# Performance work log

Hardware: AMD Instinct MI355X
Metric: run time of the kernel (lower is better)

The kernel has to match this reference:

```python
import jax, jax.numpy as jnp
import numpy as np
from jax import lax

B, T, IN, H, OUT = 4096, 512, 2, 12, 2


def setup_inputs() -> dict:
    key = jax.random.key(0)
    ks = jax.random.split(key, 11)
    s = 1.0 / np.sqrt(H)  # PyTorch LSTM init scale
    f32 = jnp.float32
    return {
        "x": jax.random.normal(ks[0], (B, T, IN), dtype=f32),
        "W_ih0": jax.random.uniform(ks[1], (4 * H, IN), dtype=f32, minval=-s, maxval=s),
        "W_hh0": jax.random.uniform(ks[2], (4 * H, H), dtype=f32, minval=-s, maxval=s),
        "b_ih0": jax.random.uniform(ks[3], (4 * H,), dtype=f32, minval=-s, maxval=s),
        "b_hh0": jax.random.uniform(ks[4], (4 * H,), dtype=f32, minval=-s, maxval=s),
        "W_ih1": jax.random.uniform(ks[5], (4 * H, H), dtype=f32, minval=-s, maxval=s),
        "W_hh1": jax.random.uniform(ks[6], (4 * H, H), dtype=f32, minval=-s, maxval=s),
        "b_ih1": jax.random.uniform(ks[7], (4 * H,), dtype=f32, minval=-s, maxval=s),
        "b_hh1": jax.random.uniform(ks[8], (4 * H,), dtype=f32, minval=-s, maxval=s),
        "fc_W": jax.random.uniform(ks[9], (OUT, H), dtype=f32, minval=-s, maxval=s),
        "fc_b": jax.random.uniform(ks[10], (OUT,), dtype=f32, minval=-s, maxval=s),
    }


def _lstm_layer(x, W_ih, W_hh, b_ih, b_hh):
    # x: [B, T, in_dim] -> hidden trajectory [B, T, H]
    b, h = x.shape[0], W_hh.shape[1]
    # Precompute input contribution for all timesteps: [T, B, 4H]
    xg = jnp.einsum('bti,gi->tbg', x, W_ih) + b_ih + b_hh

    def step(carry, xg_t):
        hprev, cprev = carry
        gates = xg_t + hprev @ W_hh.T  # [B, 4H], PyTorch gate order i,f,g,o
        i, f, g, o = jnp.split(gates, 4, axis=-1)
        i = jax.nn.sigmoid(i)
        f = jax.nn.sigmoid(f)
        g = jnp.tanh(g)
        o = jax.nn.sigmoid(o)
        c = f * cprev + i * g
        hnew = o * jnp.tanh(c)
        return (hnew, c), hnew

    z = jnp.zeros((b, h), dtype=x.dtype)
    _, hs = lax.scan(step, (z, z), xg)  # hs: [T, B, H]
    return jnp.swapaxes(hs, 0, 1)  # [B, T, H]


def reference(x, W_ih0, W_hh0, b_ih0, b_hh0, W_ih1, W_hh1, b_ih1, b_hh1, fc_W, fc_b):
    # 2-layer LSTM, h0=c0=0; dropout is identity in eval mode.
    h1 = _lstm_layer(x, W_ih0, W_hh0, b_ih0, b_hh0)   # [B, T, H]
    h2 = _lstm_layer(h1, W_ih1, W_hh1, b_ih1, b_hh1)  # [B, T, H]
    last = h2[:, -1, :]                               # [B, H]
    return last @ fc_W.T + fc_b                       # [B, OUT]
```

## Files before the change

kernel.cpp:

```cpp
#include <hip/hip_runtime.h>


namespace {
constexpr int H = 12;
constexpr int T = 512;
constexpr float LOG2E = 1.4426950408889634f;

__device__ __forceinline__ float exp2_(float x) {
    float r; asm("v_exp_f32 %0, %1" : "=v"(r) : "v"(x)); return r;
}
__device__ __forceinline__ float rcp_(float x) { return __builtin_amdgcn_rcpf(x); }
template <int CTRL>
__device__ __forceinline__ float mdpp(float v) {
    return __int_as_float(__builtin_amdgcn_mov_dpp(
        __float_as_int(v), CTRL, 0xF, 0xF, true));
}
constexpr int BC1 = 0x55;
constexpr int BC2 = 0xAA;
constexpr int BC3 = 0xFF;

__device__ __forceinline__ float tanh_(float c) {
    return fmaf(2.0f, rcp_(1.0f + exp2_(-2.0f * LOG2E * c)), -1.0f);
}
}

__global__ __launch_bounds__(512, 8) void lstm2_fc_kernel(
    const float* __restrict__ x,
    const float* __restrict__ W_ih0,
    const float* __restrict__ W_hh0,
    const float* __restrict__ b_ih0,
    const float* __restrict__ b_hh0,
    const float* __restrict__ W_ih1,
    const float* __restrict__ W_hh1,
    const float* __restrict__ b_ih1,
    const float* __restrict__ b_hh1,
    const float* __restrict__ fc_W,
    const float* __restrict__ fc_b,
    float* __restrict__ out)
{
    const int tid  = threadIdx.x;
    const int lane = tid & 63;
    const int wv   = __builtin_amdgcn_readfirstlane(tid >> 6);
    const bool L1w = (wv >= 4);
    const int ew   = wv & 3;
    const int b    = blockIdx.x * 4 + ew;
    const int u    = lane >> 2;
    const int gate = lane & 3;
    const int uc   = (u < H) ? u : 0;
    const int r    = gate * H + uc;

    const float pre  = (gate == 2) ? 2.0f : 1.0f;
    const float kmul = -LOG2E * pre;
    const float pa   = 1.0f - pre;

    __shared__ float sm[4 * 64];
    float* eb = &sm[ew * 64];
    const bool pub = (gate == 0) && (u < H);

    float w[24];
    float bias;
    if (!L1w) {
        w[0] = kmul * W_ih0[r * 2 + 0];
        w[1] = kmul * W_ih0[r * 2 + 1];
#pragma unroll
        for (int j = 0; j < H; ++j) w[2 + j] = kmul * W_hh0[r * H + j];
#pragma unroll
        for (int j = 0; j < 10; ++j) w[14 + j] = 0.0f;
        bias = kmul * (b_ih0[r] + b_hh0[r]);
    } else {
#pragma unroll
        for (int j = 0; j < H; ++j) {
            w[j]      = kmul * W_ih1[r * H + j];
            w[12 + j] = kmul * W_hh1[r * H + j];
        }
        bias = kmul * (b_ih1[r] + b_hh1[r]);
    }

    float c = 0.0f;
    float hb[H];
#pragma unroll
    for (int j = 0; j < H; ++j) hb[j] = 0.0f;

    const float* xp = x + (size_t)b * T * 2;
    float2 xc = *(const float2*)xp;

    for (int t = 0; t <= T; ++t) {
        if (!L1w) {
            if (t < T) {
                const int tn = (t < T - 1) ? (t + 1) : t;
                const float2 xn = *(const float2*)(xp + 2 * tn);
                float a = fmaf(w[0], xc.x, bias);
                a = fmaf(w[1], xc.y, a);
#pragma unroll
                for (int j = 0; j < H; ++j) a = fmaf(w[2 + j], hb[j], a);
                const float s = fmaf(pre, rcp_(1.0f + exp2_(a)), pa);
                const float F = mdpp<BC1>(s);
                const float G = mdpp<BC2>(s);
                const float O = mdpp<BC3>(s);
                c = fmaf(F, c, s * G);
                const float hv = O * tanh_(c);
                float* buf = eb + (t & 1) * 16;
                if (pub) buf[uc] = hv;
#pragma unroll
                for (int j = 0; j < H; ++j) hb[j] = buf[j];
                xc = xn;
            }
        } else {
            if (t > 0) {
                const int s0 = t - 1;
                const float* h0buf = eb + (s0 & 1) * 16;
                float a = bias;
#pragma unroll
                for (int j = 0; j < H; ++j) a = fmaf(w[12 + j], hb[j], a);
#pragma unroll
                for (int j = 0; j < H; ++j) a = fmaf(w[j], h0buf[j], a);
                const float sg = fmaf(pre, rcp_(1.0f + exp2_(a)), pa);
                const float F = mdpp<BC1>(sg);
                const float G = mdpp<BC2>(sg);
                const float O = mdpp<BC3>(sg);
                c = fmaf(F, c, sg * G);
                const float hv = O * tanh_(c);
                if (pub) eb[32 + uc] = hv;
#pragma unroll
                for (int j = 0; j < H; ++j) hb[j] = eb[32 + j];
            }
        }
        __syncthreads();
    }

    if (L1w && lane == 0) {
        float r0 = fc_b[0];
        float r1 = fc_b[1];
#pragma unroll
        for (int j = 0; j < H; ++j) {
            r0 = fmaf(fc_W[j],     hb[j], r0);
            r1 = fmaf(fc_W[H + j], hb[j], r1);
        }
        float2 res; res.x = r0; res.y = r1;
        *(float2*)(out + (size_t)b * 2) = res;
    }
}

extern "C" void kernel_launch(void* const* d_in, const int* in_sizes, int n_in,
                              void* d_out, int out_size, void* d_ws, size_t ws_size,
                              hipStream_t stream) {
    const float* x     = (const float*)d_in[0];
    const float* W_ih0 = (const float*)d_in[1];
    const float* W_hh0 = (const float*)d_in[2];
    const float* b_ih0 = (const float*)d_in[3];
    const float* b_hh0 = (const float*)d_in[4];
    const float* W_ih1 = (const float*)d_in[5];
    const float* W_hh1 = (const float*)d_in[6];
    const float* b_ih1 = (const float*)d_in[7];
    const float* b_hh1 = (const float*)d_in[8];
    const float* fc_W  = (const float*)d_in[9];
    const float* fc_b  = (const float*)d_in[10];
    float* out = (float*)d_out;

    lstm2_fc_kernel<<<1024, 512, 0, stream>>>(
        x, W_ih0, W_hh0, b_ih0, b_hh0,
        W_ih1, W_hh1, b_ih1, b_hh1, fc_W, fc_b, out);
}
```

Measured before the change: 299.0 us.

## Pack four batch rows per wave, fuse both layers, drop block barriers

Each wave now handles four batch elements, with 16 lanes per element and three hidden units per lane. One thread computes both LSTM layers in sequence, so the cross-wave __syncthreads per timestep goes away and h is shared through LDS only within the wave, ordered by a compiler memory fence. This removes the block barrier and the layer-pipelining skew, but each lane now does three times more serial FMA and transcendental work and holds many more registers. Launching 256 blocks of 256 threads with waves_per_eu 1 lowers occupancy. Correctness depends on LDS writes and reads within a wave being ordered without an explicit barrier.

```diff
diff --git a/kernel.cpp b/kernel.cpp
--- a/kernel.cpp
+++ b/kernel.cpp
@@ -10,6 +10,8 @@
     float r; asm("v_exp_f32 %0, %1" : "=v"(r) : "v"(x)); return r;
 }
 __device__ __forceinline__ float rcp_(float x) { return __builtin_amdgcn_rcpf(x); }
+__device__ __forceinline__ void memfence_() { asm volatile("" ::: "memory"); }
+
 template <int CTRL>
 __device__ __forceinline__ float mdpp(float v) {
     return __int_as_float(__builtin_amdgcn_mov_dpp(
@@ -24,7 +26,10 @@
 }
 }
 
-__global__ __launch_bounds__(512, 8) void lstm2_fc_kernel(
+__global__
+__attribute__((amdgpu_flat_work_group_size(256, 256)))
+__attribute__((amdgpu_waves_per_eu(1, 1)))
+void lstm2_fc_kernel(
     const float* __restrict__ x,
     const float* __restrict__ W_ih0,
     const float* __restrict__ W_hh0,
@@ -38,103 +43,135 @@
     const float* __restrict__ fc_b,
     float* __restrict__ out)
 {
-    const int tid  = threadIdx.x;
-    const int lane = tid & 63;
-    const int wv   = __builtin_amdgcn_readfirstlane(tid >> 6);
-    const bool L1w = (wv >= 4);
-    const int ew   = wv & 3;
-    const int b    = blockIdx.x * 4 + ew;
-    const int u    = lane >> 2;
-    const int gate = lane & 3;
-    const int uc   = (u < H) ? u : 0;
-    const int r    = gate * H + uc;
-
-    const float pre  = (gate == 2) ? 2.0f : 1.0f;
+    const int lane = threadIdx.x & 63;
+    const int wid  = __builtin_amdgcn_readfirstlane((int)threadIdx.x >> 6);
+    const int e    = lane >> 4;
+    const int s    = lane & 15;
+    const int g    = s & 3;
+    const int q    = s >> 2;
+    const int b    = blockIdx.x * 16 + wid * 4 + e;
+
+    const float pre  = (g == 2) ? 2.0f : 1.0f;
     const float kmul = -LOG2E * pre;
     const float pa   = 1.0f - pre;
 
-    __shared__ float sm[4 * 64];
-    float* eb = &sm[ew * 64];
-    const bool pub = (gate == 0) && (u < H);
-
-    float w[24];
-    float bias;
-    if (!L1w) {
-        w[0] = kmul * W_ih0[r * 2 + 0];
-        w[1] = kmul * W_ih0[r * 2 + 1];
-#pragma unroll
-        for (int j = 0; j < H; ++j) w[2 + j] = kmul * W_hh0[r * H + j];
-#pragma unroll
-        for (int j = 0; j < 10; ++j) w[14 + j] = 0.0f;
-        bias = kmul * (b_ih0[r] + b_hh0[r]);
-    } else {
+    __shared__ __align__(16) float sm[384];
+    float* h0row = &sm[(wid * 4 + e) * 12];
+    float* h1row = &sm[192 + (wid * 4 + e) * 12];
+    const bool pub = (g == 0);
+
+    float wx0[3], wx1[3], bias0[3], bias1[3];
+    float whh0[3][H], wih1[3][H], whh1[3][H];
+#pragma unroll
+    for (int Tt = 0; Tt < 3; ++Tt) {
+        const int r = g * H + (q + 4 * Tt);
+        wx0[Tt]   = kmul * W_ih0[r * 2 + 0];
+        wx1[Tt]   = kmul * W_ih0[r * 2 + 1];
+        bias0[Tt] = kmul * (b_ih0[r] + b_hh0[r]);
+        bias1[Tt] = kmul * (b_ih1[r] + b_hh1[r]);
 #pragma unroll
         for (int j = 0; j < H; ++j) {
-            w[j]      = kmul * W_ih1[r * H + j];
-            w[12 + j] = kmul * W_hh1[r * H + j];
-        }
-        bias = kmul * (b_ih1[r] + b_hh1[r]);
+            whh0[Tt][j] = kmul * W_hh0[r * H + j];
+            wih1[Tt][j] = kmul * W_ih1[r * H + j];
+            whh1[Tt][j] = kmul * W_hh1[r * H + j];
+        }
     }
 
-    float c = 0.0f;
-    float hb[H];
-#pragma unroll
-    for (int j = 0; j < H; ++j) hb[j] = 0.0f;
+    float c0[3] = {0.0f, 0.0f, 0.0f};
+    float c1[3] = {0.0f, 0.0f, 0.0f};
+    float h0b[H], h1b[H];
+#pragma unroll
+    for (int j = 0; j < H; ++j) { h0b[j] = 0.0f; h1b[j] = 0.0f; }
 
     const float* xp = x + (size_t)b * T * 2;
     float2 xc = *(const float2*)xp;
 
-    for (int t = 0; t <= T; ++t) {
-        if (!L1w) {
-            if (t < T) {
-                const int tn = (t < T - 1) ? (t + 1) : t;
-                const float2 xn = *(const float2*)(xp + 2 * tn);
-                float a = fmaf(w[0], xc.x, bias);
-                a = fmaf(w[1], xc.y, a);
-#pragma unroll
-                for (int j = 0; j < H; ++j) a = fmaf(w[2 + j], hb[j], a);
-                const float s = fmaf(pre, rcp_(1.0f + exp2_(a)), pa);
-                const float F = mdpp<BC1>(s);
-                const float G = mdpp<BC2>(s);
-                const float O = mdpp<BC3>(s);
-                c = fmaf(F, c, s * G);
-                const float hv = O * tanh_(c);
-                float* buf = eb + (t & 1) * 16;
-                if (pub) buf[uc] = hv;
-#pragma unroll
-                for (int j = 0; j < H; ++j) hb[j] = buf[j];
-                xc = xn;
-            }
-        } else {
-            if (t > 0) {
-                const int s0 = t - 1;
-                const float* h0buf = eb + (s0 & 1) * 16;
-                float a = bias;
-#pragma unroll
-                for (int j = 0; j < H; ++j) a = fmaf(w[12 + j], hb[j], a);
-#pragma unroll
-                for (int j = 0; j < H; ++j) a = fmaf(w[j], h0buf[j], a);
-                const float sg = fmaf(pre, rcp_(1.0f + exp2_(a)), pa);
-                const float F = mdpp<BC1>(sg);
-                const float G = mdpp<BC2>(sg);
-                const float O = mdpp<BC3>(sg);
-                c = fmaf(F, c, sg * G);
-                const float hv = O * tanh_(c);
-                if (pub) eb[32 + uc] = hv;
-#pragma unroll
-                for (int j = 0; j < H; ++j) hb[j] = eb[32 + j];
-            }
-        }
-        __syncthreads();
+    for (int t = 0; t < T; ++t) {
+        const int tn = (t < T - 1) ? (t + 1) : t;
+        const float2 xn = *(const float2*)(xp + 2 * tn);
+
+        float a0[3];
+#pragma unroll
+        for (int Tt = 0; Tt < 3; ++Tt) {
+            float acc = fmaf(wx0[Tt], xc.x, bias0[Tt]);
+            acc = fmaf(wx1[Tt], xc.y, acc);
+#pragma unroll
+            for (int j = 0; j < H; ++j) acc = fmaf(whh0[Tt][j], h0b[j], acc);
+            a0[Tt] = acc;
+        }
+        float h0v[3];
+#pragma unroll
+        for (int Tt = 0; Tt < 3; ++Tt) {
+            const float sv = fmaf(pre, rcp_(1.0f + exp2_(a0[Tt])), pa);
+            const float Fv = mdpp<BC1>(sv);
+            const float Gv = mdpp<BC2>(sv);
+            const float Ov = mdpp<BC3>(sv);
+            c0[Tt] = fmaf(Fv, c0[Tt], sv * Gv);
+            h0v[Tt] = Ov * tanh_(c0[Tt]);
+        }
+        if (pub) {
+            h0row[q + 0] = h0v[0];
+            h0row[q + 4] = h0v[1];
+            h0row[q + 8] = h0v[2];
+        }
+        float a1[3];
+#pragma unroll
+        for (int Tt = 0; Tt < 3; ++Tt) {
+            float acc = bias1[Tt];
+#pragma unroll
+            for (int j = 0; j < H; ++j) acc = fmaf(whh1[Tt][j], h1b[j], acc);
+            a1[Tt] = acc;
+        }
+        memfence_();
+        {
+            const float4 r0 = *(const float4*)(h0row + 0);
+            const float4 r1 = *(const float4*)(h0row + 4);
+            const float4 r2 = *(const float4*)(h0row + 8);
+            h0b[0] = r0.x; h0b[1] = r0.y; h0b[2]  = r0.z; h0b[3]  = r0.w;
+            h0b[4] = r1.x; h0b[5] = r1.y; h0b[6]  = r1.z; h0b[7]  = r1.w;
+            h0b[8] = r2.x; h0b[9] = r2.y; h0b[10] = r2.z; h0b[11] = r2.w;
+        }
+#pragma unroll
+        for (int Tt = 0; Tt < 3; ++Tt) {
+            float acc = a1[Tt];
+#pragma unroll
+            for (int j = 0; j < H; ++j) acc = fmaf(wih1[Tt][j], h0b[j], acc);
+            a1[Tt] = acc;
+        }
+        float h1v[3];
+#pragma unroll
+        for (int Tt = 0; Tt < 3; ++Tt) {
+            const float sv = fmaf(pre, rcp_(1.0f + exp2_(a1[Tt])), pa);
+            const float Fv = mdpp<BC1>(sv);
+            const float Gv = mdpp<BC2>(sv);
+            const float Ov = mdpp<BC3>(sv);
+            c1[Tt] = fmaf(Fv, c1[Tt], sv * Gv);
+            h1v[Tt] = Ov * tanh_(c1[Tt]);
+        }
+        if (pub) {
+            h1row[q + 0] = h1v[0];
+            h1row[q + 4] = h1v[1];
+            h1row[q + 8] = h1v[2];
+        }
+        memfence_();
+        {
+            const float4 r0 = *(const float4*)(h1row + 0);
+            const float4 r1 = *(const float4*)(h1row + 4);
+            const float4 r2 = *(const float4*)(h1row + 8);
+            h1b[0] = r0.x; h1b[1] = r0.y; h1b[2]  = r0.z; h1b[3]  = r0.w;
+            h1b[4] = r1.x; h1b[5] = r1.y; h1b[6]  = r1.z; h1b[7]  = r1.w;
+            h1b[8] = r2.x; h1b[9] = r2.y; h1b[10] = r2.z; h1b[11] = r2.w;
+        }
+        xc = xn;
     }
 
-    if (L1w && lane == 0) {
+    if (s == 0) {
         float r0 = fc_b[0];
         float r1 = fc_b[1];
 #pragma unroll
         for (int j = 0; j < H; ++j) {
-            r0 = fmaf(fc_W[j],     hb[j], r0);
-            r1 = fmaf(fc_W[H + j], hb[j], r1);
+            r0 = fmaf(fc_W[j],     h1b[j], r0);
+            r1 = fmaf(fc_W[H + j], h1b[j], r1);
         }
         float2 res; res.x = r0; res.y = r1;
         *(float2*)(out + (size_t)b * 2) = res;
@@ -157,7 +194,7 @@
     const float* fc_b  = (const float*)d_in[10];
     float* out = (float*)d_out;
 
-    lstm2_fc_kernel<<<1024, 512, 0, stream>>>(
+    lstm2_fc_kernel<<<256, 256, 0, stream>>>(
         x, W_ih0, W_hh0, b_ih0, b_hh0,
         W_ih1, W_hh1, b_ih1, b_hh1, fc_W, fc_b, out);
 }
```

Result: faster. 283.0 us (-5.3%).

## Pack four batch elements per wavefront with three hidden units per lane

Applied to the files above, without the earlier changes.

Remaps lanes so each wavefront handles four batch elements in 16-lane groups, each lane computing three hidden units across the gate quartet. This removes idle lanes and shrinks the grid to 256 blocks, with vectorized float4 LDS reads of the hidden state. In exchange, each lane runs three times the serial FMA work per timestep and far fewer waves are resident, so latency hiding relies on ILP across the three chains.

```diff
diff --git a/kernel.cpp b/kernel.cpp
--- a/kernel.cpp
+++ b/kernel.cpp
@@ -10,6 +10,8 @@
     float r; asm("v_exp_f32 %0, %1" : "=v"(r) : "v"(x)); return r;
 }
 __device__ __forceinline__ float rcp_(float x) { return __builtin_amdgcn_rcpf(x); }
+__device__ __forceinline__ void memfence_() { asm volatile("" ::: "memory"); }
+
 template <int CTRL>
 __device__ __forceinline__ float mdpp(float v) {
     return __int_as_float(__builtin_amdgcn_mov_dpp(
@@ -24,7 +26,7 @@
 }
 }
 
-__global__ __launch_bounds__(512, 8) void lstm2_fc_kernel(
+__global__ __launch_bounds__(512, 2) void lstm2_fc_kernel(
     const float* __restrict__ x,
     const float* __restrict__ W_ih0,
     const float* __restrict__ W_hh0,
@@ -42,93 +44,145 @@
     const int lane = tid & 63;
     const int wv   = __builtin_amdgcn_readfirstlane(tid >> 6);
     const bool L1w = (wv >= 4);
-    const int ew   = wv & 3;
-    const int b    = blockIdx.x * 4 + ew;
-    const int u    = lane >> 2;
-    const int gate = lane & 3;
-    const int uc   = (u < H) ? u : 0;
-    const int r    = gate * H + uc;
-
-    const float pre  = (gate == 2) ? 2.0f : 1.0f;
+    const int eg   = wv & 3;
+    const int e    = lane >> 4;
+    const int s    = lane & 15;
+    const int g    = s & 3;
+    const int q    = s >> 2;
+    const int el   = eg * 4 + e;
+    const int b    = blockIdx.x * 16 + el;
+
+    const float pre  = (g == 2) ? 2.0f : 1.0f;
     const float kmul = -LOG2E * pre;
     const float pa   = 1.0f - pre;
 
-    __shared__ float sm[4 * 64];
-    float* eb = &sm[ew * 64];
-    const bool pub = (gate == 0) && (u < H);
-
-    float w[24];
-    float bias;
+    __shared__ float sm[16 * 48];
+    float* eb = &sm[el * 48];
+    const bool pub = (g == 0);
+
+    float wx0c[3], wx1c[3], bias[3];
+    float wA[3][H], wB[3][H];
     if (!L1w) {
-        w[0] = kmul * W_ih0[r * 2 + 0];
-        w[1] = kmul * W_ih0[r * 2 + 1];
-#pragma unroll
-        for (int j = 0; j < H; ++j) w[2 + j] = kmul * W_hh0[r * H + j];
-#pragma unroll
-        for (int j = 0; j < 10; ++j) w[14 + j] = 0.0f;
-        bias = kmul * (b_ih0[r] + b_hh0[r]);
+#pragma unroll
+        for (int Tt = 0; Tt < 3; ++Tt) {
+            const int r = g * H + (q + 4 * Tt);
+            wx0c[Tt] = kmul * W_ih0[r * 2 + 0];
+            wx1c[Tt] = kmul * W_ih0[r * 2 + 1];
+            bias[Tt] = kmul * (b_ih0[r] + b_hh0[r]);
+#pragma unroll
+            for (int j = 0; j < H; ++j) {
+                wA[Tt][j] = kmul * W_hh0[r * H + j];
+                wB[Tt][j] = 0.0f;
+            }
+        }
     } else {
 #pragma unroll
-        for (int j = 0; j < H; ++j) {
-            w[j]      = kmul * W_ih1[r * H + j];
-            w[12 + j] = kmul * W_hh1[r * H + j];
-        }
-        bias = kmul * (b_ih1[r] + b_hh1[r]);
+        for (int Tt = 0; Tt < 3; ++Tt) {
+            const int r = g * H + (q + 4 * Tt);
+            wx0c[Tt] = 0.0f; wx1c[Tt] = 0.0f;
+            bias[Tt] = kmul * (b_ih1[r] + b_hh1[r]);
+#pragma unroll
+            for (int j = 0; j < H; ++j) {
+                wA[Tt][j] = kmul * W_ih1[r * H + j];
+                wB[Tt][j] = kmul * W_hh1[r * H + j];
+            }
+        }
     }
 
-    float c = 0.0f;
+    float c[3] = {0.0f, 0.0f, 0.0f};
     float hb[H];
 #pragma unroll
     for (int j = 0; j < H; ++j) hb[j] = 0.0f;
 
     const float* xp = x + (size_t)b * T * 2;
-    float2 xc = *(const float2*)xp;
+    float2 xc; xc.x = 0.0f; xc.y = 0.0f;
+    if (!L1w) xc = *(const float2*)xp;
 
     for (int t = 0; t <= T; ++t) {
         if (!L1w) {
             if (t < T) {
                 const int tn = (t < T - 1) ? (t + 1) : t;
                 const float2 xn = *(const float2*)(xp + 2 * tn);
-                float a = fmaf(w[0], xc.x, bias);
-                a = fmaf(w[1], xc.y, a);
-#pragma unroll
-                for (int j = 0; j < H; ++j) a = fmaf(w[2 + j], hb[j], a);
-                const float s = fmaf(pre, rcp_(1.0f + exp2_(a)), pa);
-                const float F = mdpp<BC1>(s);
-                const float G = mdpp<BC2>(s);
-                const float O = mdpp<BC3>(s);
-                c = fmaf(F, c, s * G);
-                const float hv = O * tanh_(c);
+                float a[3];
+#pragma unroll
+                for (int Tt = 0; Tt < 3; ++Tt) {
+                    float acc = fmaf(wx0c[Tt], xc.x, bias[Tt]);
+                    acc = fmaf(wx1c[Tt], xc.y, acc);
+#pragma unroll
+                    for (int j = 0; j < H; ++j) acc = fmaf(wA[Tt][j], hb[j], acc);
+                    a[Tt] = acc;
+                }
+                float hv[3];
+#pragma unroll
+                for (int Tt = 0; Tt < 3; ++Tt) {
+                    const float sv = fmaf(pre, rcp_(1.0f + exp2_(a[Tt])), pa);
+                    const float Fv = mdpp<BC1>(sv);
+                    const float Gv = mdpp<BC2>(sv);
+                    const float Ov = mdpp<BC3>(sv);
+                    c[Tt] = fmaf(Fv, c[Tt], sv * Gv);
+                    hv[Tt] = Ov * tanh_(c[Tt]);
+                }
                 float* buf = eb + (t & 1) * 16;
-                if (pub) buf[uc] = hv;
-#pragma unroll
-                for (int j = 0; j < H; ++j) hb[j] = buf[j];
+                if (pub) { buf[q] = hv[0]; buf[q + 4] = hv[1]; buf[q + 8] = hv[2]; }
+                memfence_();
+                {
+                    const float4 r0 = *(const float4*)(buf + 0);
+                    const float4 r1 = *(const float4*)(buf + 4);
+                    const float4 r2 = *(const float4*)(buf + 8);
+                    hb[0] = r0.x; hb[1] = r0.y; hb[2]  = r0.z; hb[3]  = r0.w;
+                    hb[4] = r1.x; hb[5] = r1.y; hb[6]  = r1.z; hb[7]  = r1.w;
+                    hb[8] = r2.x; hb[9] = r2.y; hb[10] = r2.z; hb[11] = r2.w;
+                }
                 xc = xn;
             }
         } else {
             if (t > 0) {
-                const int s0 = t - 1;
-                const float* h0buf = eb + (s0 & 1) * 16;
-                float a = bias;
-#pragma unroll
-                for (int j = 0; j < H; ++j) a = fmaf(w[12 + j], hb[j], a);
-#pragma unroll
-                for (int j = 0; j < H; ++j) a = fmaf(w[j], h0buf[j], a);
-                const float sg = fmaf(pre, rcp_(1.0f + exp2_(a)), pa);
-                const float F = mdpp<BC1>(sg);
-                const float G = mdpp<BC2>(sg);
-                const float O = mdpp<BC3>(sg);
-                c = fmaf(F, c, sg * G);
-                const float hv = O * tanh_(c);
-                if (pub) eb[32 + uc] = hv;
-#pragma unroll
-                for (int j = 0; j < H; ++j) hb[j] = eb[32 + j];
+                const float* h0buf = eb + ((t - 1) & 1) * 16;
+                float h0v_[H];
+                {
+                    const float4 r0 = *(const float4*)(h0buf + 0);
+                    const float4 r1 = *(const float4*)(h0buf + 4);
+                    const float4 r2 = *(const float4*)(h0buf + 8);
+                    h0v_[0] = r0.x; h0v_[1] = r0.y; h0v_[2]  = r0.z; h0v_[3]  = r0.w;
+                    h0v_[4] = r1.x; h0v_[5] = r1.y; h0v_[6]  = r1.z; h0v_[7]  = r1.w;
+                    h0v_[8] = r2.x; h0v_[9] = r2.y; h0v_[10] = r2.z; h0v_[11] = r2.w;
+                }
+                float a[3];
+#pragma unroll
+                for (int Tt = 0; Tt < 3; ++Tt) {
+                    float acc = bias[Tt];
+#pragma unroll
+                    for (int j = 0; j < H; ++j) acc = fmaf(wB[Tt][j], hb[j], acc);
+#pragma unroll
+                    for (int j = 0; j < H; ++j) acc = fmaf(wA[Tt][j], h0v_[j], acc);
+                    a[Tt] = acc;
+                }
+                float hv[3];
+#pragma unroll
+                for (int Tt = 0; Tt < 3; ++Tt) {
+                    const float sv = fmaf(pre, rcp_(1.0f + exp2_(a[Tt])), pa);
+                    const float Fv = mdpp<BC1>(sv);
+                    const float Gv = mdpp<BC2>(sv);
+                    const float Ov = mdpp<BC3>(sv);
+                    c[Tt] = fmaf(Fv, c[Tt], sv * Gv);
+                    hv[Tt] = Ov * tanh_(c[Tt]);
+                }
+                if (pub) { eb[32 + q] = hv[0]; eb[36 + q] = hv[1]; eb[40 + q] = hv[2]; }
+                memfence_();
+                {
+                    const float4 r0 = *(const float4*)(eb + 32);
+                    const float4 r1 = *(const float4*)(eb + 36);
+                    const float4 r2 = *(const float4*)(eb + 40);
+                    hb[0] = r0.x; hb[1] = r0.y; hb[2]  = r0.z; hb[3]  = r0.w;
+                    hb[4] = r1.x; hb[5] = r1.y; hb[6]  = r1.z; hb[7]  = r1.w;
+                    hb[8] = r2.x; hb[9] = r2.y; hb[10] = r2.z; hb[11] = r2.w;
+                }
             }
         }
         __syncthreads();
     }
 
-    if (L1w && lane == 0) {
+    if (L1w && s == 0) {
         float r0 = fc_b[0];
         float r1 = fc_b[1];
 #pragma unroll
@@ -157,7 +211,7 @@
     const float* fc_b  = (const float*)d_in[10];
     float* out = (float*)d_out;
 
-    lstm2_fc_kernel<<<1024, 512, 0, stream>>>(
+    lstm2_fc_kernel<<<256, 512, 0, stream>>>(
         x, W_ih0, W_hh0, b_ih0, b_hh0,
         W_ih1, W_hh1, b_ih1, b_hh1, fc_W, fc_b, out);
 }
```

New measurement: 268.8 us. 1.11x faster.
